# Kernel tuning notes

Hardware: AMD Instinct MI355X
Metric: run time of the kernel (lower is better)

## Reference

```python
import jax, jax.numpy as jnp
import numpy as np

N_AGENTS = 512
OBS = 128          # embed_fc_input_size (args.obs_space)
INP = 656          # input_shape
HID = 64           # rnn_hidden_dim
LAT = 256          # latent_dim (hard-coded)
NH = 64            # NN_HIDDEN_SIZE (hard-coded)
VAR_FLOOR = 0.002
KL_W = 1e-4
H_W = 1e-4
SOFT_W = 1.0
BN_EPS = 1e-5
LOG2PI = float(np.log(2.0 * np.pi))


def _bn(x, g, b, axis):
    # BatchNorm1d in training mode: biased batch stats over `axis`
    m = x.mean(axis=axis, keepdims=True)
    v = x.var(axis=axis, keepdims=True)
    return g * (x - m) / jnp.sqrt(v + BN_EPS) + b


def setup_inputs() -> dict:
    key = jax.random.key(0)
    ks = jax.random.split(key, 12)
    s = 0.02  # small init so exp(log-var head) stays tame
    p = {}
    p["obs"] = jax.random.normal(ks[0], (N_AGENTS, INP), jnp.float32)
    p["hidden_state"] = jax.random.normal(ks[1], (N_AGENTS, HID), jnp.float32)
    p["eps"] = jax.random.normal(ks[2], (N_AGENTS, LAT), jnp.float32)

    def lin(k, din, dout):
        return jax.random.normal(k, (din, dout), jnp.float32) * s, jnp.zeros((dout,), jnp.float32)

    # embed_net: Linear(OBS,64) -> BN -> LeakyReLU -> Linear(64, 2*LAT)
    p["eW1"], p["eb1"] = lin(ks[3], OBS, NH)
    p["eg"], p["ebt"] = jnp.ones((NH,), jnp.float32), jnp.zeros((NH,), jnp.float32)
    p["eW2"], p["eb2"] = lin(ks[4], NH, 2 * LAT)
    # inference_net: Linear(HID+INP,64) -> BN -> LeakyReLU -> Linear(64, 2*LAT)
    p["iW1"], p["ib1"] = lin(ks[5], HID + INP, NH)
    p["ig"], p["ibt"] = jnp.ones((NH,), jnp.float32), jnp.zeros((NH,), jnp.float32)
    p["iW2"], p["ib2"] = lin(ks[6], NH, 2 * LAT)
    # dis_net: Linear(2*LAT,64) -> BN -> LeakyReLU -> Linear(64,1)
    p["dW1"], p["db1"] = lin(ks[7], 2 * LAT, NH)
    p["dg"], p["dbt"] = jnp.ones((NH,), jnp.float32), jnp.zeros((NH,), jnp.float32)
    p["dW2"], p["db2"] = lin(ks[8], NH, 1)
    return p


def reference(obs, hidden_state, eps,
              eW1, eb1, eg, ebt, eW2, eb2,
              iW1, ib1, ig, ibt, iW2, ib2,
              dW1, db1, dg, dbt, dW2, db2):
    n = N_AGENTS  # bs == 1 is hard-coded in the module
    # --- embed_net ---
    emb_in = obs[:, -OBS:]
    h = jax.nn.leaky_relu(_bn(emb_in @ eW1 + eb1, eg, ebt, axis=0))
    lat = h @ eW2 + eb2                       # [n, 2*LAT]
    mu = lat[:, :LAT]
    var = jnp.maximum(jnp.exp(lat[:, LAT:]), VAR_FLOOR)
    sig = jnp.sqrt(var)
    latent = mu + sig * eps                   # rsample

    # --- inference_net (h_in detached) ---
    inf_in = jnp.concatenate([jax.lax.stop_gradient(hidden_state), obs], axis=1)
    hi = jax.nn.leaky_relu(_bn(inf_in @ iW1 + ib1, ig, ibt, axis=0))
    li = hi @ iW2 + ib2
    mu_q = li[:, :LAT]
    var_q = jnp.maximum(jnp.exp(li[:, LAT:]), VAR_FLOOR)
    sig_q = jnp.sqrt(var_q)

    entropy = (0.5 + 0.5 * LOG2PI + jnp.log(sig)).sum(-1).mean()
    kl = (jnp.log(sig_q / sig) + (var + (mu - mu_q) ** 2) / (2.0 * var_q) - 0.5).sum(-1).mean()
    loss0 = jnp.minimum(entropy * H_W + kl * KL_W, 2000.0)
    ce_loss = jnp.log1p(jnp.exp(loss0))

    # --- vectorized ring-shift pairwise pass (replaces n_agents Python loop) ---
    shifts = jnp.arange(1, n + 1)                        # loop iterations 1..n
    idx = (jnp.arange(n)[None, :] - shifts[:, None]) % n  # [n_shifts, n]
    moved = latent[idx]                                   # [S, n, LAT]

    # mi: per-dim Normal(mu_j, sig_j).log_prob of shifted latents
    logp = -((moved - mu[None]) ** 2) / (2.0 * var[None]) - jnp.log(sig)[None] - 0.5 * LOG2PI
    mi = jnp.maximum(logp + 13.9, -13.9).sum(-1) / LAT    # [S, n]

    # dis_net on concat(latent_j, moved_{s,j}); BN stats per shift iteration (batch = n)
    pair = jnp.concatenate([jnp.broadcast_to(latent[None], (n, n, LAT)), moved], axis=-1)
    h1 = pair @ dW1 + db1                                 # [S, n, NH]
    h1 = jax.nn.leaky_relu(_bn(h1, dg, dbt, axis=1))
    dis = jnp.abs(h1 @ dW2 + db2)[..., 0]                 # [S, n]

    mi_cat = mi.reshape(1, -1)                            # shift-major, matches cat order
    dis_cat = dis.reshape(1, -1)

    mi_n = (mi_cat - mi_cat.min(1, keepdims=True)) / (mi_cat.max(1, keepdims=True) - mi_cat.min(1, keepdims=True) + 1e-12)
    dis_n = (dis_cat - dis_cat.min(1, keepdims=True)) / (dis_cat.max(1, keepdims=True) - dis_cat.min(1, keepdims=True) + 1e-12)

    dis_loss = -jnp.minimum(mi_n + dis_n, 1.0).sum() / n  # / bs / n_agents, bs=1
    dis_norm = jnp.abs(dis_n).sum(axis=1).sum() / n
    c_dis_loss = (dis_norm + SOFT_W * dis_loss) / n
    loss = ce_loss + c_dis_loss
    return loss, c_dis_loss, ce_loss
```

## Files before the change

kernel.cpp:

```cpp
#include <hip/hip_runtime.h>

#define LOG2PI_F 1.8378770664093453f

#define W_ENC_PRE 0
#define W_INF_PRE 32768
#define W_ACC     65536
#define W_FIN     65792
#define W_MIMM    65796
#define W_DSMM    66308
#define W_ENT     67332
#define W_KL      67588
#define W_LATENT  67844
#define W_RPC     198916
#define W_A       723204
#define W_B       755972
#define W_AT      788740
#define W_BT      821508
#define W_ALPHA   854276
#define W_BETA    887044
#define W_MI      919812
#define W_DIS     1181956

__global__ __launch_bounds__(256) void k_pre(
    const float* __restrict__ obs, const float* __restrict__ hid,
    const float* __restrict__ eW1, const float* __restrict__ iW1,
    float* __restrict__ enc_pre, float* __restrict__ inf_pre,
    float* __restrict__ acc) {
  __shared__ float x[2][720];
  __shared__ float pi[4][2][64];
  __shared__ float pe[4][2][64];
  const int t = threadIdx.x;
  const int i0 = blockIdx.x * 2;
#pragma unroll
  for (int r = 0; r < 2; ++r)
    for (int k = t; k < 720; k += 256)
      x[r][k] = (k < 64) ? hid[(i0 + r) * 64 + k] : obs[(i0 + r) * 656 + (k - 64)];
  __syncthreads();
  const int c = t & 63, q = t >> 6;
  {
    float a0 = 0.f, a1 = 0.f;
    const int k0 = q * 180;
    for (int k = k0; k < k0 + 180; ++k) {
      const float w = iW1[k * 64 + c];
      a0 = fmaf(x[0][k], w, a0);
      a1 = fmaf(x[1][k], w, a1);
    }
    pi[q][0][c] = a0;
    pi[q][1][c] = a1;
  }
  {
    float a0 = 0.f, a1 = 0.f;
    const int k0 = q * 32;
    for (int k = k0; k < k0 + 32; ++k) {
      const float w = eW1[k * 64 + c];
      a0 = fmaf(x[0][592 + k], w, a0);
      a1 = fmaf(x[1][592 + k], w, a1);
    }
    pe[q][0][c] = a0;
    pe[q][1][c] = a1;
  }
  __syncthreads();
  if (t < 128) {
    const int r = t >> 6, c2 = t & 63;
    const float s = pi[0][r][c2] + pi[1][r][c2] + pi[2][r][c2] + pi[3][r][c2];
    inf_pre[(i0 + r) * 64 + c2] = s;
    atomicAdd(&acc[128 + c2], s);
    atomicAdd(&acc[192 + c2], s * s);
  } else {
    const int r = (t >> 6) & 1, c2 = t & 63;
    const float s = pe[0][r][c2] + pe[1][r][c2] + pe[2][r][c2] + pe[3][r][c2];
    enc_pre[(i0 + r) * 64 + c2] = s;
    atomicAdd(&acc[c2], s);
    atomicAdd(&acc[64 + c2], s * s);
  }
}

__global__ __launch_bounds__(256) void k_lat(
    const float* __restrict__ enc_pre, const float* __restrict__ inf_pre,
    const float* __restrict__ acc, const float* __restrict__ eg,
    const float* __restrict__ ebt, const float* __restrict__ ig,
    const float* __restrict__ ibt, const float* __restrict__ eW2,
    const float* __restrict__ eb2, const float* __restrict__ iW2,
    const float* __restrict__ ib2, const float* __restrict__ eps,
    float* __restrict__ latent, float* __restrict__ rpc,
    float* __restrict__ ent_part, float* __restrict__ kl_part) {
  __shared__ float sc[2][64], sh[2][64];
  __shared__ float h[2][2][64];
  __shared__ float red[256];
  const int t = threadIdx.x;
  const int i0 = blockIdx.x * 2;
  if (t < 128) {
    const int w = t >> 6, c = t & 63;
    const float sum = acc[w * 128 + c], sq = acc[w * 128 + 64 + c];
    const float mean = sum * (1.f / 512.f);
    float var = sq * (1.f / 512.f) - mean * mean;
    var = fmaxf(var, 0.f);
    const float g = w ? ig[c] : eg[c];
    const float bt = w ? ibt[c] : ebt[c];
    const float scale = g * rsqrtf(var + 1e-5f);
    sc[w][c] = scale;
    sh[w][c] = bt - mean * scale;
  }
  __syncthreads();
  {
    const int w = t >> 7, r = (t >> 6) & 1, c = t & 63;
    const float* pre = w ? inf_pre : enc_pre;
    const float v = fmaf(pre[(i0 + r) * 64 + c], sc[w][c], sh[w][c]);
    h[w][r][c] = (v >= 0.f) ? v : 0.01f * v;
  }
  __syncthreads();
  float me[2] = {0.f, 0.f}, ve[2] = {0.f, 0.f};
  float mq[2] = {0.f, 0.f}, vq[2] = {0.f, 0.f};
  for (int c = 0; c < 64; ++c) {
    const float we1 = eW2[c * 512 + t], we2 = eW2[c * 512 + 256 + t];
    const float wi1 = iW2[c * 512 + t], wi2 = iW2[c * 512 + 256 + t];
#pragma unroll
    for (int r = 0; r < 2; ++r) {
      me[r] = fmaf(h[0][r][c], we1, me[r]);
      ve[r] = fmaf(h[0][r][c], we2, ve[r]);
      mq[r] = fmaf(h[1][r][c], wi1, mq[r]);
      vq[r] = fmaf(h[1][r][c], wi2, vq[r]);
    }
  }
  const float ebm = eb2[t], ebv = eb2[256 + t];
  const float ibm = ib2[t], ibv = ib2[256 + t];
  float ent_l = 0.f, kl_l = 0.f;
#pragma unroll
  for (int r = 0; r < 2; ++r) {
    const int i = i0 + r;
    const float m = me[r] + ebm;
    const float var = fmaxf(expf(ve[r] + ebv), 0.002f);
    const float lse = 0.5f * logf(var);
    const float sig = sqrtf(var);
    const float mqq = mq[r] + ibm;
    const float varq = fmaxf(expf(vq[r] + ibv), 0.002f);
    const float lsq = 0.5f * logf(varq);
    latent[i * 256 + t] = fmaf(sig, eps[i * 256 + t], m);
    const float r_ = sqrtf(0.5f / var);
    float4 o;
    o.x = r_;
    o.y = m * r_;
    o.z = 13.9f - 0.5f * LOG2PI_F - lse;
    o.w = 0.f;
    *(float4*)&rpc[(i * 256 + t) * 4] = o;
    ent_l += 0.5f + 0.5f * LOG2PI_F + lse;
    const float dmu = m - mqq;
    kl_l += lsq - lse + (var + dmu * dmu) * (0.5f / varq) - 0.5f;
  }
  red[t] = ent_l;
  __syncthreads();
  for (int o = 128; o; o >>= 1) {
    if (t < o) red[t] += red[t + o];
    __syncthreads();
  }
  if (t == 0) ent_part[blockIdx.x] = red[0];
  __syncthreads();
  red[t] = kl_l;
  __syncthreads();
  for (int o = 128; o; o >>= 1) {
    if (t < o) red[t] += red[t + o];
    __syncthreads();
  }
  if (t == 0) kl_part[blockIdx.x] = red[0];
}

__global__ __launch_bounds__(256) void k_AB(
    const float* __restrict__ latent, const float* __restrict__ dW1,
    float* __restrict__ A, float* __restrict__ B, float* __restrict__ At,
    float* __restrict__ Bt, float* __restrict__ fin) {
  if (blockIdx.x == 0 && threadIdx.x == 0) {
    fin[0] = 0.f;
    fin[1] = 0.f;
    ((unsigned*)fin)[2] = 0u;
  }
  __shared__ float ls[2][256];
  __shared__ float pA[4][2][64], pB[4][2][64];
  const int t = threadIdx.x;
  const int j0 = blockIdx.x * 2;
  ls[0][t] = latent[j0 * 256 + t];
  ls[1][t] = latent[(j0 + 1) * 256 + t];
  __syncthreads();
  const int c = t & 63, q = t >> 6;
  float aA0 = 0.f, aA1 = 0.f, aB0 = 0.f, aB1 = 0.f;
  const int k0 = q * 64;
  for (int k = k0; k < k0 + 64; ++k) {
    const float wA = dW1[k * 64 + c];
    const float wB = dW1[(256 + k) * 64 + c];
    aA0 = fmaf(ls[0][k], wA, aA0);
    aA1 = fmaf(ls[1][k], wA, aA1);
    aB0 = fmaf(ls[0][k], wB, aB0);
    aB1 = fmaf(ls[1][k], wB, aB1);
  }
  pA[q][0][c] = aA0;
  pA[q][1][c] = aA1;
  pB[q][0][c] = aB0;
  pB[q][1][c] = aB1;
  __syncthreads();
  if (t < 128) {
    const int r = t >> 6, c2 = t & 63;
    const float s = pA[0][r][c2] + pA[1][r][c2] + pA[2][r][c2] + pA[3][r][c2];
    A[(j0 + r) * 64 + c2] = s;
    At[c2 * 512 + j0 + r] = s;
  } else {
    const int r = (t >> 6) & 1, c2 = t & 63;
    const float s = pB[0][r][c2] + pB[1][r][c2] + pB[2][r][c2] + pB[3][r][c2];
    B[(j0 + r) * 64 + c2] = s;
    Bt[c2 * 512 + j0 + r] = s;
  }
}

__global__ __launch_bounds__(256) void k_cross(
    const float* __restrict__ At, const float* __restrict__ Bt,
    const float* __restrict__ dg, const float* __restrict__ dbt,
    float* __restrict__ alpha, float* __restrict__ beta) {
  __shared__ float a[512], bb[512];
  __shared__ float red[256];
  __shared__ float pc[4][64];
  const int t = threadIdx.x;
  const int c = blockIdx.x >> 3;
  const int s0 = (blockIdx.x & 7) * 64;
  const float a0 = At[c * 512 + t], a1 = At[c * 512 + 256 + t];
  const float b0 = Bt[c * 512 + t], b1 = Bt[c * 512 + 256 + t];
  a[t] = a0;
  a[t + 256] = a1;
  bb[t] = b0;
  bb[t + 256] = b1;
  red[t] = a0 + a1 + b0 + b1;
  __syncthreads();
  for (int o = 128; o; o >>= 1) {
    if (t < o) red[t] += red[t + o];
    __syncthreads();
  }
  const float S = red[0];
  __syncthreads();
  red[t] = a0 * a0 + a1 * a1 + b0 * b0 + b1 * b1;
  __syncthreads();
  for (int o = 128; o; o >>= 1) {
    if (t < o) red[t] += red[t + o];
    __syncthreads();
  }
  const float Q = red[0];
  const int sl = t & 63, part = t >> 6;
  const int s = s0 + sl;
  float cr = 0.f;
  for (int j = part * 128; j < part * 128 + 128; ++j)
    cr = fmaf(a[j], bb[(j - s - 1) & 511], cr);
  pc[part][sl] = cr;
  __syncthreads();
  if (t < 64) {
    const int ss = s0 + t;
    const float cross = pc[0][t] + pc[1][t] + pc[2][t] + pc[3][t];
    const float mean = S * (1.f / 512.f);
    const float var = (Q + 2.f * cross) * (1.f / 512.f) - mean * mean;
    const float gc = dg[c], bc = dbt[c];
    const float al = rsqrtf(var + 1e-5f) * gc;
    alpha[ss * 64 + c] = al;
    beta[ss * 64 + c] = bc - mean * al;
  }
}

__global__ __launch_bounds__(256) void k_mi(
    const float* __restrict__ latent, const float* __restrict__ rpc,
    float* __restrict__ mi, float2* __restrict__ miMM) {
  __shared__ float lats[64][65];
  __shared__ float rpcs[16 * 256];
  __shared__ float mt[64][17];
  __shared__ float fmn[256], fmx[256];
  const int t = threadIdx.x;
  const int jt = blockIdx.x & 31, pt = blockIdx.x >> 5;
  const int j0 = jt * 16, p0 = pt * 64;
  const int pl = t & 31, jg = t >> 5;
  float regL[16], regR[16];
#pragma unroll
  for (int i = 0; i < 16; ++i) {
    const int idx = t + i * 256;
    regL[i] = latent[(p0 + (idx >> 6)) * 256 + (idx & 63)];
    regR[i] = rpc[(j0 + (idx >> 8)) * 1024 + (idx & 255)];
  }
  float a00 = 0.f, a01 = 0.f, a10 = 0.f, a11 = 0.f;
  for (int kc = 0; kc < 4; ++kc) {
    __syncthreads();
#pragma unroll
    for (int i = 0; i < 16; ++i) {
      const int idx = t + i * 256;
      lats[idx >> 6][idx & 63] = regL[i];
      rpcs[idx] = regR[i];
    }
    __syncthreads();
    if (kc < 3) {
#pragma unroll
      for (int i = 0; i < 16; ++i) {
        const int idx = t + i * 256;
        regL[i] = latent[(p0 + (idx >> 6)) * 256 + (kc + 1) * 64 + (idx & 63)];
        regR[i] = rpc[(j0 + (idx >> 8)) * 1024 + (kc + 1) * 256 + (idx & 255)];
      }
    }
    const float4* rp0 = (const float4*)&rpcs[(jg * 2) * 256];
    const float4* rp1 = (const float4*)&rpcs[(jg * 2 + 1) * 256];
#pragma unroll 8
    for (int k = 0; k < 64; ++k) {
      const float l0 = lats[pl][k], l1 = lats[pl + 32][k];
      const float4 r0 = rp0[k];
      const float4 r1 = rp1[k];
      float v;
      v = fmaf(l0, r0.x, -r0.y);
      a00 += fmaxf(fmaf(-v, v, r0.z), -13.9f);
      v = fmaf(l1, r0.x, -r0.y);
      a01 += fmaxf(fmaf(-v, v, r0.z), -13.9f);
      v = fmaf(l0, r1.x, -r1.y);
      a10 += fmaxf(fmaf(-v, v, r1.z), -13.9f);
      v = fmaf(l1, r1.x, -r1.y);
      a11 += fmaxf(fmaf(-v, v, r1.z), -13.9f);
    }
  }
  a00 *= (1.f / 256.f);
  a01 *= (1.f / 256.f);
  a10 *= (1.f / 256.f);
  a11 *= (1.f / 256.f);
  __syncthreads();
  mt[pl][jg * 2] = a00;
  mt[pl + 32][jg * 2] = a01;
  mt[pl][jg * 2 + 1] = a10;
  mt[pl + 32][jg * 2 + 1] = a11;
  fmn[t] = fminf(fminf(a00, a01), fminf(a10, a11));
  fmx[t] = fmaxf(fmaxf(a00, a01), fmaxf(a10, a11));
  __syncthreads();
  for (int o = 128; o; o >>= 1) {
    if (t < o) {
      fmn[t] = fminf(fmn[t], fmn[t + o]);
      fmx[t] = fmaxf(fmx[t], fmx[t + o]);
    }
    __syncthreads();
  }
  if (t == 0) miMM[blockIdx.x] = make_float2(fmn[0], fmx[0]);
  for (int i = t; i < 1024; i += 256) {
    const int pr = i >> 4, jc = i & 15;
    mi[(p0 + pr) * 512 + (j0 + jc)] = mt[pr][jc];
  }
}

__global__ __launch_bounds__(256) void k_dis(
    const float* __restrict__ A, const float* __restrict__ B,
    const float* __restrict__ alpha, const float* __restrict__ beta,
    const float* __restrict__ dW2, const float* __restrict__ db2,
    float* __restrict__ dis, float2* __restrict__ dsMM) {
  __shared__ float As[8 * 66];
  __shared__ float Bs[64 * 66];
  __shared__ float als[71 * 66];
  __shared__ float bes[71 * 66];
  __shared__ float w2s[64];
  __shared__ float dt[64][9];
  __shared__ float fmn[256], fmx[256];
  const int t = threadIdx.x;
  const int jt = blockIdx.x & 63, pt = blockIdx.x >> 6;
  const int j0 = jt * 8, p0 = pt * 64;
  for (int idx = t; idx < 8 * 64; idx += 256)
    As[(idx >> 6) * 66 + (idx & 63)] = A[(j0 + (idx >> 6)) * 64 + (idx & 63)];
  for (int idx = t; idx < 64 * 64; idx += 256)
    Bs[(idx >> 6) * 66 + (idx & 63)] = B[(p0 + (idx >> 6)) * 64 + (idx & 63)];
  for (int idx = t; idx < 71 * 64; idx += 256) {
    const int r = idx >> 6, c = idx & 63;
    const int s = (j0 - p0 - 64 + r) & 511;
    als[r * 66 + c] = alpha[s * 64 + c];
    bes[r * 66 + c] = beta[s * 64 + c];
  }
  if (t < 64) w2s[t] = dW2[t];
  const float db2v = db2[0];
  __syncthreads();
  const int pl = t & 31, jg = t >> 5;
  const int rb0 = jg - pl + 63;
  const int rb1 = jg - pl + 31;
  float acc0 = 0.f, acc1 = 0.f;
  for (int c = 0; c < 64; c += 2) {
    const float2 av = *(const float2*)&As[jg * 66 + c];
    const float2 bv0 = *(const float2*)&Bs[pl * 66 + c];
    const float2 bv1 = *(const float2*)&Bs[(pl + 32) * 66 + c];
    const float2 al0 = *(const float2*)&als[rb0 * 66 + c];
    const float2 al1 = *(const float2*)&als[rb1 * 66 + c];
    const float2 be0 = *(const float2*)&bes[rb0 * 66 + c];
    const float2 be1 = *(const float2*)&bes[rb1 * 66 + c];
    const float2 w = *(const float2*)&w2s[c];
    float v;
    v = fmaf(av.x + bv0.x, al0.x, be0.x);
    v = (v >= 0.f) ? v : 0.01f * v;
    acc0 = fmaf(v, w.x, acc0);
    v = fmaf(av.y + bv0.y, al0.y, be0.y);
    v = (v >= 0.f) ? v : 0.01f * v;
    acc0 = fmaf(v, w.y, acc0);
    v = fmaf(av.x + bv1.x, al1.x, be1.x);
    v = (v >= 0.f) ? v : 0.01f * v;
    acc1 = fmaf(v, w.x, acc1);
    v = fmaf(av.y + bv1.y, al1.y, be1.y);
    v = (v >= 0.f) ? v : 0.01f * v;
    acc1 = fmaf(v, w.y, acc1);
  }
  acc0 = fabsf(acc0 + db2v);
  acc1 = fabsf(acc1 + db2v);
  dt[pl][jg] = acc0;
  dt[pl + 32][jg] = acc1;
  fmn[t] = fminf(acc0, acc1);
  fmx[t] = fmaxf(acc0, acc1);
  __syncthreads();
  for (int o = 128; o; o >>= 1) {
    if (t < o) {
      fmn[t] = fminf(fmn[t], fmn[t + o]);
      fmx[t] = fmaxf(fmx[t], fmx[t + o]);
    }
    __syncthreads();
  }
  if (t == 0) dsMM[blockIdx.x] = make_float2(fmn[0], fmx[0]);
  for (int idx = t; idx < 512; idx += 256) {
    const int pr = idx >> 3, jc = idx & 7;
    dis[(p0 + pr) * 512 + (j0 + jc)] = dt[pr][jc];
  }
}

__global__ __launch_bounds__(256) void k_sumfin(
    const float* __restrict__ mi, const float* __restrict__ dis,
    const float2* __restrict__ miMM, const float2* __restrict__ dsMM,
    float* __restrict__ fin, const float* __restrict__ ent_part,
    const float* __restrict__ kl_part, float* __restrict__ out) {
  __shared__ float red1[256], red2[256], red3[256], red4[256];
  __shared__ int lastflag;
  const int t = threadIdx.x;
  {
    const float2 v = miMM[t];
    const float2 w0 = dsMM[t], w1 = dsMM[t + 256];
    red1[t] = v.x;
    red2[t] = v.y;
    red3[t] = fminf(w0.x, w1.x);
    red4[t] = fmaxf(w0.y, w1.y);
  }
  __syncthreads();
  for (int o = 128; o; o >>= 1) {
    if (t < o) {
      red1[t] = fminf(red1[t], red1[t + o]);
      red2[t] = fmaxf(red2[t], red2[t + o]);
      red3[t] = fminf(red3[t], red3[t + o]);
      red4[t] = fmaxf(red4[t], red4[t + o]);
    }
    __syncthreads();
  }
  const float mi_mn = red1[0], mi_mx = red2[0];
  const float d_mn = red3[0], d_mx = red4[0];
  __syncthreads();
  const float inv_mi = 1.f / (mi_mx - mi_mn + 1e-12f);
  const float inv_d = 1.f / (d_mx - d_mn + 1e-12f);
  float s1 = 0.f, s2 = 0.f;
  for (int i = blockIdx.x * 256 + t; i < 512 * 512; i += 65536) {
    const float mn_ = (mi[i] - mi_mn) * inv_mi;
    const float dn_ = (dis[i] - d_mn) * inv_d;
    s1 += fminf(mn_ + dn_, 1.0f);
    s2 += dn_;
  }
  red1[t] = s1;
  red2[t] = s2;
  __syncthreads();
  for (int o = 128; o; o >>= 1) {
    if (t < o) {
      red1[t] += red1[t + o];
      red2[t] += red2[t + o];
    }
    __syncthreads();
  }
  if (t == 0) {
    atomicAdd(&fin[0], red1[0]);
    atomicAdd(&fin[1], red2[0]);
    __threadfence();
    const unsigned old = atomicAdd((unsigned*)&fin[2], 1u);
    lastflag = (old == 255u) ? 1 : 0;
  }
  __syncthreads();
  if (!lastflag) return;
  red1[t] = ent_part[t];
  red2[t] = kl_part[t];
  __syncthreads();
  for (int o = 128; o; o >>= 1) {
    if (t < o) {
      red1[t] += red1[t + o];
      red2[t] += red2[t + o];
    }
    __syncthreads();
  }
  if (t == 0) {
    const float S1 = atomicAdd(&fin[0], 0.f);
    const float S2 = atomicAdd(&fin[1], 0.f);
    const double entropy = (double)red1[0] / 512.0;
    const double kl = (double)red2[0] / 512.0;
    double l0 = entropy * 1e-4 + kl * 1e-4;
    if (l0 > 2000.0) l0 = 2000.0;
    const double ce = log1p(exp(l0));
    const double dis_loss = -(double)S1 / 512.0;
    const double dis_norm = (double)S2 / 512.0;
    const double c_dis = (dis_norm + dis_loss) / 512.0;
    out[0] = (float)(ce + c_dis);
    out[1] = (float)c_dis;
    out[2] = (float)ce;
  }
}

extern "C" void kernel_launch(void* const* d_in, const int* in_sizes, int n_in,
                              void* d_out, int out_size, void* d_ws,
                              size_t ws_size, hipStream_t stream) {
  (void)in_sizes;
  (void)n_in;
  (void)out_size;
  (void)ws_size;
  const float* obs = (const float*)d_in[0];
  const float* hid = (const float*)d_in[1];
  const float* eps = (const float*)d_in[2];
  const float* eW1 = (const float*)d_in[3];
  const float* eg = (const float*)d_in[5];
  const float* ebt = (const float*)d_in[6];
  const float* eW2 = (const float*)d_in[7];
  const float* eb2 = (const float*)d_in[8];
  const float* iW1 = (const float*)d_in[9];
  const float* ig = (const float*)d_in[11];
  const float* ibt = (const float*)d_in[12];
  const float* iW2 = (const float*)d_in[13];
  const float* ib2 = (const float*)d_in[14];
  const float* dW1 = (const float*)d_in[15];
  const float* dg = (const float*)d_in[17];
  const float* dbt = (const float*)d_in[18];
  const float* dW2 = (const float*)d_in[19];
  const float* db2 = (const float*)d_in[20];
  float* ws = (float*)d_ws;
  float* out = (float*)d_out;

  hipMemsetAsync(ws + W_ACC, 0, 256 * sizeof(float), stream);

  k_pre<<<256, 256, 0, stream>>>(obs, hid, eW1, iW1, ws + W_ENC_PRE,
                                 ws + W_INF_PRE, ws + W_ACC);
  k_lat<<<256, 256, 0, stream>>>(ws + W_ENC_PRE, ws + W_INF_PRE, ws + W_ACC, eg,
                                 ebt, ig, ibt, eW2, eb2, iW2, ib2, eps,
                                 ws + W_LATENT, ws + W_RPC, ws + W_ENT,
                                 ws + W_KL);
  k_AB<<<256, 256, 0, stream>>>(ws + W_LATENT, dW1, ws + W_A, ws + W_B,
                                ws + W_AT, ws + W_BT, ws + W_FIN);
  k_cross<<<512, 256, 0, stream>>>(ws + W_AT, ws + W_BT, dg, dbt, ws + W_ALPHA,
                                   ws + W_BETA);
  k_mi<<<256, 256, 0, stream>>>(ws + W_LATENT, ws + W_RPC, ws + W_MI,
                                (float2*)(ws + W_MIMM));
  k_dis<<<512, 256, 0, stream>>>(ws + W_A, ws + W_B, ws + W_ALPHA, ws + W_BETA,
                                 dW2, db2, ws + W_DIS, (float2*)(ws + W_DSMM));
  k_sumfin<<<256, 256, 0, stream>>>(ws + W_MI, ws + W_DIS,
                                    (const float2*)(ws + W_MIMM),
                                    (const float2*)(ws + W_DSMM), ws + W_FIN,
                                    ws + W_ENT, ws + W_KL, out);
}
```

Before: 201.2 us.

## Fuse all stages into one cooperative megakernel with grid syncs

Replaces seven separate kernel launches and a memset with a single cooperative kernel of 512 blocks. Stages are separated by grid.sync and each block handles one row or tile. This removes launch and inter-kernel gaps, and the final atomic last-block reduction is replaced by per-block partials reduced after a grid sync. The cost is grid-wide barrier overhead, and occupancy is capped by the requirement that all 512 blocks be co-resident (launch bounds of 2 blocks per CU, large shared array).

Result: slower. 617.0 us (+206.7%).

```diff
diff --git a/kernel.cpp b/kernel.cpp
--- a/kernel.cpp
+++ b/kernel.cpp
@@ -1,501 +1,500 @@
 #include <hip/hip_runtime.h>
+#include <hip/hip_cooperative_groups.h>
+
+namespace cg = cooperative_groups;
 
 #define LOG2PI_F 1.8378770664093453f
 
 #define W_ENC_PRE 0
 #define W_INF_PRE 32768
 #define W_ACC     65536
-#define W_FIN     65792
-#define W_MIMM    65796
-#define W_DSMM    66308
-#define W_ENT     67332
-#define W_KL      67588
-#define W_LATENT  67844
-#define W_RPC     198916
-#define W_A       723204
-#define W_B       755972
-#define W_AT      788740
-#define W_BT      821508
-#define W_ALPHA   854276
-#define W_BETA    887044
-#define W_MI      919812
-#define W_DIS     1181956
-
-__global__ __launch_bounds__(256) void k_pre(
-    const float* __restrict__ obs, const float* __restrict__ hid,
-    const float* __restrict__ eW1, const float* __restrict__ iW1,
-    float* __restrict__ enc_pre, float* __restrict__ inf_pre,
-    float* __restrict__ acc) {
-  __shared__ float x[2][720];
-  __shared__ float pi[4][2][64];
-  __shared__ float pe[4][2][64];
+#define W_ENT     65792
+#define W_KL      66304
+#define W_MIMM    66816
+#define W_DSMM    67840
+#define W_S1P     68864
+#define W_S2P     69376
+#define W_LATENT  69888
+#define W_RPC     200960
+#define W_A       725248
+#define W_B       758016
+#define W_AT      790784
+#define W_BT      823552
+#define W_ALPHA   856320
+#define W_BETA    889088
+#define W_MI      921856
+#define W_DIS     1184000
+
+struct Params {
+  const float *obs, *hid, *eps;
+  const float *eW1, *eg, *ebt, *eW2, *eb2;
+  const float *iW1, *ig, *ibt, *iW2, *ib2;
+  const float *dW1, *dg, *dbt, *dW2, *db2;
+  float* ws;
+  float* out;
+};
+
+__global__ __launch_bounds__(256, 2) void megak(Params p) {
+  __shared__ __align__(16) float sm[15276];
+  cg::grid_group grid = cg::this_grid();
   const int t = threadIdx.x;
-  const int i0 = blockIdx.x * 2;
-#pragma unroll
-  for (int r = 0; r < 2; ++r)
+  const int vb = blockIdx.x;
+  float* ws = p.ws;
+  float* acc = ws + W_ACC;
+
+  if (vb == 0) acc[t] = 0.f;
+  grid.sync();
+
+  {
+    float* xs = sm;
+    float* pi = sm + 720;
+    float* pe = sm + 976;
+    const int i = vb;
     for (int k = t; k < 720; k += 256)
-      x[r][k] = (k < 64) ? hid[(i0 + r) * 64 + k] : obs[(i0 + r) * 656 + (k - 64)];
-  __syncthreads();
-  const int c = t & 63, q = t >> 6;
-  {
-    float a0 = 0.f, a1 = 0.f;
-    const int k0 = q * 180;
-    for (int k = k0; k < k0 + 180; ++k) {
-      const float w = iW1[k * 64 + c];
-      a0 = fmaf(x[0][k], w, a0);
-      a1 = fmaf(x[1][k], w, a1);
-    }
-    pi[q][0][c] = a0;
-    pi[q][1][c] = a1;
-  }
-  {
-    float a0 = 0.f, a1 = 0.f;
-    const int k0 = q * 32;
-    for (int k = k0; k < k0 + 32; ++k) {
-      const float w = eW1[k * 64 + c];
-      a0 = fmaf(x[0][592 + k], w, a0);
-      a1 = fmaf(x[1][592 + k], w, a1);
-    }
-    pe[q][0][c] = a0;
-    pe[q][1][c] = a1;
-  }
-  __syncthreads();
-  if (t < 128) {
-    const int r = t >> 6, c2 = t & 63;
-    const float s = pi[0][r][c2] + pi[1][r][c2] + pi[2][r][c2] + pi[3][r][c2];
-    inf_pre[(i0 + r) * 64 + c2] = s;
-    atomicAdd(&acc[128 + c2], s);
-    atomicAdd(&acc[192 + c2], s * s);
-  } else {
-    const int r = (t >> 6) & 1, c2 = t & 63;
-    const float s = pe[0][r][c2] + pe[1][r][c2] + pe[2][r][c2] + pe[3][r][c2];
-    enc_pre[(i0 + r) * 64 + c2] = s;
-    atomicAdd(&acc[c2], s);
-    atomicAdd(&acc[64 + c2], s * s);
-  }
-}
-
-__global__ __launch_bounds__(256) void k_lat(
-    const float* __restrict__ enc_pre, const float* __restrict__ inf_pre,
-    const float* __restrict__ acc, const float* __restrict__ eg,
-    const float* __restrict__ ebt, const float* __restrict__ ig,
-    const float* __restrict__ ibt, const float* __restrict__ eW2,
-    const float* __restrict__ eb2, const float* __restrict__ iW2,
-    const float* __restrict__ ib2, const float* __restrict__ eps,
-    float* __restrict__ latent, float* __restrict__ rpc,
-    float* __restrict__ ent_part, float* __restrict__ kl_part) {
-  __shared__ float sc[2][64], sh[2][64];
-  __shared__ float h[2][2][64];
-  __shared__ float red[256];
-  const int t = threadIdx.x;
-  const int i0 = blockIdx.x * 2;
-  if (t < 128) {
-    const int w = t >> 6, c = t & 63;
-    const float sum = acc[w * 128 + c], sq = acc[w * 128 + 64 + c];
-    const float mean = sum * (1.f / 512.f);
-    float var = sq * (1.f / 512.f) - mean * mean;
-    var = fmaxf(var, 0.f);
-    const float g = w ? ig[c] : eg[c];
-    const float bt = w ? ibt[c] : ebt[c];
-    const float scale = g * rsqrtf(var + 1e-5f);
-    sc[w][c] = scale;
-    sh[w][c] = bt - mean * scale;
-  }
-  __syncthreads();
-  {
-    const int w = t >> 7, r = (t >> 6) & 1, c = t & 63;
-    const float* pre = w ? inf_pre : enc_pre;
-    const float v = fmaf(pre[(i0 + r) * 64 + c], sc[w][c], sh[w][c]);
-    h[w][r][c] = (v >= 0.f) ? v : 0.01f * v;
-  }
-  __syncthreads();
-  float me[2] = {0.f, 0.f}, ve[2] = {0.f, 0.f};
-  float mq[2] = {0.f, 0.f}, vq[2] = {0.f, 0.f};
-  for (int c = 0; c < 64; ++c) {
-    const float we1 = eW2[c * 512 + t], we2 = eW2[c * 512 + 256 + t];
-    const float wi1 = iW2[c * 512 + t], wi2 = iW2[c * 512 + 256 + t];
-#pragma unroll
-    for (int r = 0; r < 2; ++r) {
-      me[r] = fmaf(h[0][r][c], we1, me[r]);
-      ve[r] = fmaf(h[0][r][c], we2, ve[r]);
-      mq[r] = fmaf(h[1][r][c], wi1, mq[r]);
-      vq[r] = fmaf(h[1][r][c], wi2, vq[r]);
-    }
-  }
-  const float ebm = eb2[t], ebv = eb2[256 + t];
-  const float ibm = ib2[t], ibv = ib2[256 + t];
-  float ent_l = 0.f, kl_l = 0.f;
-#pragma unroll
-  for (int r = 0; r < 2; ++r) {
-    const int i = i0 + r;
-    const float m = me[r] + ebm;
-    const float var = fmaxf(expf(ve[r] + ebv), 0.002f);
+      xs[k] = (k < 64) ? p.hid[i * 64 + k] : p.obs[i * 656 + (k - 64)];
+    __syncthreads();
+    const int c = t & 63, q = t >> 6;
+    {
+      float a0 = 0.f;
+      const int k0 = q * 180;
+      for (int k = k0; k < k0 + 180; ++k)
+        a0 = fmaf(xs[k], p.iW1[k * 64 + c], a0);
+      pi[q * 64 + c] = a0;
+    }
+    {
+      float a0 = 0.f;
+      const int k0 = q * 32;
+      for (int k = k0; k < k0 + 32; ++k)
+        a0 = fmaf(xs[592 + k], p.eW1[k * 64 + c], a0);
+      pe[q * 64 + c] = a0;
+    }
+    __syncthreads();
+    if (t < 64) {
+      const float s = pi[t] + pi[64 + t] + pi[128 + t] + pi[192 + t];
+      (ws + W_INF_PRE)[i * 64 + t] = s;
+      atomicAdd(&acc[128 + t], s);
+      atomicAdd(&acc[192 + t], s * s);
+    } else if (t < 128) {
+      const int c2 = t - 64;
+      const float s = pe[c2] + pe[64 + c2] + pe[128 + c2] + pe[192 + c2];
+      (ws + W_ENC_PRE)[i * 64 + c2] = s;
+      atomicAdd(&acc[c2], s);
+      atomicAdd(&acc[64 + c2], s * s);
+    }
+  }
+  grid.sync();
+
+  {
+    float* sc = sm;
+    float* sh = sm + 128;
+    float* h2 = sm + 256;
+    float* red = sm + 384;
+    const int i = vb;
+    if (t < 128) {
+      const int w = t >> 6, c = t & 63;
+      const float sum = acc[w * 128 + c], sq = acc[w * 128 + 64 + c];
+      const float mean = sum * (1.f / 512.f);
+      float var = sq * (1.f / 512.f) - mean * mean;
+      var = fmaxf(var, 0.f);
+      const float g = w ? p.ig[c] : p.eg[c];
+      const float bt = w ? p.ibt[c] : p.ebt[c];
+      const float scale = g * rsqrtf(var + 1e-5f);
+      sc[w * 64 + c] = scale;
+      sh[w * 64 + c] = bt - mean * scale;
+    }
+    __syncthreads();
+    if (t < 128) {
+      const int w = t >> 6, c = t & 63;
+      const float* pre = w ? (ws + W_INF_PRE) : (ws + W_ENC_PRE);
+      const float v = fmaf(pre[i * 64 + c], sc[w * 64 + c], sh[w * 64 + c]);
+      h2[w * 64 + c] = (v >= 0.f) ? v : 0.01f * v;
+    }
+    __syncthreads();
+    float me = 0.f, ve = 0.f, mq = 0.f, vq = 0.f;
+    for (int c = 0; c < 64; ++c) {
+      const float he = h2[c], hq = h2[64 + c];
+      me = fmaf(he, p.eW2[c * 512 + t], me);
+      ve = fmaf(he, p.eW2[c * 512 + 256 + t], ve);
+      mq = fmaf(hq, p.iW2[c * 512 + t], mq);
+      vq = fmaf(hq, p.iW2[c * 512 + 256 + t], vq);
+    }
+    const float m = me + p.eb2[t];
+    const float var = fmaxf(expf(ve + p.eb2[256 + t]), 0.002f);
     const float lse = 0.5f * logf(var);
     const float sig = sqrtf(var);
-    const float mqq = mq[r] + ibm;
-    const float varq = fmaxf(expf(vq[r] + ibv), 0.002f);
+    const float mqq = mq + p.ib2[t];
+    const float varq = fmaxf(expf(vq + p.ib2[256 + t]), 0.002f);
     const float lsq = 0.5f * logf(varq);
-    latent[i * 256 + t] = fmaf(sig, eps[i * 256 + t], m);
+    (ws + W_LATENT)[i * 256 + t] = fmaf(sig, p.eps[i * 256 + t], m);
     const float r_ = sqrtf(0.5f / var);
     float4 o;
     o.x = r_;
     o.y = m * r_;
     o.z = 13.9f - 0.5f * LOG2PI_F - lse;
     o.w = 0.f;
-    *(float4*)&rpc[(i * 256 + t) * 4] = o;
-    ent_l += 0.5f + 0.5f * LOG2PI_F + lse;
+    *(float4*)&(ws + W_RPC)[(i * 256 + t) * 4] = o;
+    const float ent_l = 0.5f + 0.5f * LOG2PI_F + lse;
     const float dmu = m - mqq;
-    kl_l += lsq - lse + (var + dmu * dmu) * (0.5f / varq) - 0.5f;
-  }
-  red[t] = ent_l;
-  __syncthreads();
-  for (int o = 128; o; o >>= 1) {
-    if (t < o) red[t] += red[t + o];
-    __syncthreads();
-  }
-  if (t == 0) ent_part[blockIdx.x] = red[0];
-  __syncthreads();
-  red[t] = kl_l;
-  __syncthreads();
-  for (int o = 128; o; o >>= 1) {
-    if (t < o) red[t] += red[t + o];
-    __syncthreads();
-  }
-  if (t == 0) kl_part[blockIdx.x] = red[0];
-}
-
-__global__ __launch_bounds__(256) void k_AB(
-    const float* __restrict__ latent, const float* __restrict__ dW1,
-    float* __restrict__ A, float* __restrict__ B, float* __restrict__ At,
-    float* __restrict__ Bt, float* __restrict__ fin) {
-  if (blockIdx.x == 0 && threadIdx.x == 0) {
-    fin[0] = 0.f;
-    fin[1] = 0.f;
-    ((unsigned*)fin)[2] = 0u;
-  }
-  __shared__ float ls[2][256];
-  __shared__ float pA[4][2][64], pB[4][2][64];
-  const int t = threadIdx.x;
-  const int j0 = blockIdx.x * 2;
-  ls[0][t] = latent[j0 * 256 + t];
-  ls[1][t] = latent[(j0 + 1) * 256 + t];
-  __syncthreads();
-  const int c = t & 63, q = t >> 6;
-  float aA0 = 0.f, aA1 = 0.f, aB0 = 0.f, aB1 = 0.f;
-  const int k0 = q * 64;
-  for (int k = k0; k < k0 + 64; ++k) {
-    const float wA = dW1[k * 64 + c];
-    const float wB = dW1[(256 + k) * 64 + c];
-    aA0 = fmaf(ls[0][k], wA, aA0);
-    aA1 = fmaf(ls[1][k], wA, aA1);
-    aB0 = fmaf(ls[0][k], wB, aB0);
-    aB1 = fmaf(ls[1][k], wB, aB1);
-  }
-  pA[q][0][c] = aA0;
-  pA[q][1][c] = aA1;
-  pB[q][0][c] = aB0;
-  pB[q][1][c] = aB1;
-  __syncthreads();
-  if (t < 128) {
-    const int r = t >> 6, c2 = t & 63;
-    const float s = pA[0][r][c2] + pA[1][r][c2] + pA[2][r][c2] + pA[3][r][c2];
-    A[(j0 + r) * 64 + c2] = s;
-    At[c2 * 512 + j0 + r] = s;
-  } else {
-    const int r = (t >> 6) & 1, c2 = t & 63;
-    const float s = pB[0][r][c2] + pB[1][r][c2] + pB[2][r][c2] + pB[3][r][c2];
-    B[(j0 + r) * 64 + c2] = s;
-    Bt[c2 * 512 + j0 + r] = s;
-  }
-}
-
-__global__ __launch_bounds__(256) void k_cross(
-    const float* __restrict__ At, const float* __restrict__ Bt,
-    const float* __restrict__ dg, const float* __restrict__ dbt,
-    float* __restrict__ alpha, float* __restrict__ beta) {
-  __shared__ float a[512], bb[512];
-  __shared__ float red[256];
-  __shared__ float pc[4][64];
-  const int t = threadIdx.x;
-  const int c = blockIdx.x >> 3;
-  const int s0 = (blockIdx.x & 7) * 64;
-  const float a0 = At[c * 512 + t], a1 = At[c * 512 + 256 + t];
-  const float b0 = Bt[c * 512 + t], b1 = Bt[c * 512 + 256 + t];
-  a[t] = a0;
-  a[t + 256] = a1;
-  bb[t] = b0;
-  bb[t + 256] = b1;
-  red[t] = a0 + a1 + b0 + b1;
-  __syncthreads();
-  for (int o = 128; o; o >>= 1) {
-    if (t < o) red[t] += red[t + o];
-    __syncthreads();
-  }
-  const float S = red[0];
-  __syncthreads();
-  red[t] = a0 * a0 + a1 * a1 + b0 * b0 + b1 * b1;
-  __syncthreads();
-  for (int o = 128; o; o >>= 1) {
-    if (t < o) red[t] += red[t + o];
-    __syncthreads();
-  }
-  const float Q = red[0];
-  const int sl = t & 63, part = t >> 6;
-  const int s = s0 + sl;
-  float cr = 0.f;
-  for (int j = part * 128; j < part * 128 + 128; ++j)
-    cr = fmaf(a[j], bb[(j - s - 1) & 511], cr);
-  pc[part][sl] = cr;
-  __syncthreads();
-  if (t < 64) {
-    const int ss = s0 + t;
-    const float cross = pc[0][t] + pc[1][t] + pc[2][t] + pc[3][t];
-    const float mean = S * (1.f / 512.f);
-    const float var = (Q + 2.f * cross) * (1.f / 512.f) - mean * mean;
-    const float gc = dg[c], bc = dbt[c];
-    const float al = rsqrtf(var + 1e-5f) * gc;
-    alpha[ss * 64 + c] = al;
-    beta[ss * 64 + c] = bc - mean * al;
-  }
-}
-
-__global__ __launch_bounds__(256) void k_mi(
-    const float* __restrict__ latent, const float* __restrict__ rpc,
-    float* __restrict__ mi, float2* __restrict__ miMM) {
-  __shared__ float lats[64][65];
-  __shared__ float rpcs[16 * 256];
-  __shared__ float mt[64][17];
-  __shared__ float fmn[256], fmx[256];
-  const int t = threadIdx.x;
-  const int jt = blockIdx.x & 31, pt = blockIdx.x >> 5;
-  const int j0 = jt * 16, p0 = pt * 64;
-  const int pl = t & 31, jg = t >> 5;
-  float regL[16], regR[16];
-#pragma unroll
-  for (int i = 0; i < 16; ++i) {
-    const int idx = t + i * 256;
-    regL[i] = latent[(p0 + (idx >> 6)) * 256 + (idx & 63)];
-    regR[i] = rpc[(j0 + (idx >> 8)) * 1024 + (idx & 255)];
-  }
-  float a00 = 0.f, a01 = 0.f, a10 = 0.f, a11 = 0.f;
-  for (int kc = 0; kc < 4; ++kc) {
-    __syncthreads();
+    const float kl_l = lsq - lse + (var + dmu * dmu) * (0.5f / varq) - 0.5f;
+    red[t] = ent_l;
+    __syncthreads();
+    for (int o2 = 128; o2; o2 >>= 1) {
+      if (t < o2) red[t] += red[t + o2];
+      __syncthreads();
+    }
+    if (t == 0) (ws + W_ENT)[i] = red[0];
+    __syncthreads();
+    red[t] = kl_l;
+    __syncthreads();
+    for (int o2 = 128; o2; o2 >>= 1) {
+      if (t < o2) red[t] += red[t + o2];
+      __syncthreads();
+    }
+    if (t == 0) (ws + W_KL)[i] = red[0];
+  }
+  grid.sync();
+
+  {
+    float* ls = sm;
+    float* pA = sm + 256;
+    float* pB = sm + 512;
+    const int i = vb;
+    ls[t] = (ws + W_LATENT)[i * 256 + t];
+    __syncthreads();
+    const int c = t & 63, q = t >> 6;
+    float aA = 0.f, aB = 0.f;
+    const int k0 = q * 64;
+    for (int k = k0; k < k0 + 64; ++k) {
+      const float x = ls[k];
+      aA = fmaf(x, p.dW1[k * 64 + c], aA);
+      aB = fmaf(x, p.dW1[(256 + k) * 64 + c], aB);
+    }
+    pA[q * 64 + c] = aA;
+    pB[q * 64 + c] = aB;
+    __syncthreads();
+    if (t < 64) {
+      const float s = pA[t] + pA[64 + t] + pA[128 + t] + pA[192 + t];
+      (ws + W_A)[i * 64 + t] = s;
+      (ws + W_AT)[t * 512 + i] = s;
+    } else if (t < 128) {
+      const int c2 = t - 64;
+      const float s = pB[c2] + pB[64 + c2] + pB[128 + c2] + pB[192 + c2];
+      (ws + W_B)[i * 64 + c2] = s;
+      (ws + W_BT)[c2 * 512 + i] = s;
+    }
+  }
+  grid.sync();
+
+  {
+    float* a = sm;
+    float* bb = sm + 512;
+    float* red = sm + 1024;
+    float* pc = sm + 1280;
+    const int c = vb >> 3;
+    const int s0 = (vb & 7) * 64;
+    const float* At = ws + W_AT;
+    const float* Bt = ws + W_BT;
+    const float a0 = At[c * 512 + t], a1 = At[c * 512 + 256 + t];
+    const float b0 = Bt[c * 512 + t], b1 = Bt[c * 512 + 256 + t];
+    a[t] = a0;
+    a[t + 256] = a1;
+    bb[t] = b0;
+    bb[t + 256] = b1;
+    red[t] = a0 + a1 + b0 + b1;
+    __syncthreads();
+    for (int o = 128; o; o >>= 1) {
+      if (t < o) red[t] += red[t + o];
+      __syncthreads();
+    }
+    const float S = red[0];
+    __syncthreads();
+    red[t] = a0 * a0 + a1 * a1 + b0 * b0 + b1 * b1;
+    __syncthreads();
+    for (int o = 128; o; o >>= 1) {
+      if (t < o) red[t] += red[t + o];
+      __syncthreads();
+    }
+    const float Q = red[0];
+    const int sl = t & 63, part = t >> 6;
+    const int s = s0 + sl;
+    float cr = 0.f;
+    for (int j = part * 128; j < part * 128 + 128; ++j)
+      cr = fmaf(a[j], bb[(j - s - 1) & 511], cr);
+    pc[part * 64 + sl] = cr;
+    __syncthreads();
+    if (t < 64) {
+      const int ss = s0 + t;
+      const float cross = pc[t] + pc[64 + t] + pc[128 + t] + pc[192 + t];
+      const float mean = S * (1.f / 512.f);
+      const float var = (Q + 2.f * cross) * (1.f / 512.f) - mean * mean;
+      const float gc = p.dg[c], bc = p.dbt[c];
+      const float al = rsqrtf(var + 1e-5f) * gc;
+      (ws + W_ALPHA)[ss * 64 + c] = al;
+      (ws + W_BETA)[ss * 64 + c] = bc - mean * al;
+    }
+  }
+  grid.sync();
+
+  {
+    float* lats = sm;
+    float* rpcs = sm + 4160;
+    float* mt = sm + 6208;
+    float* fmn = sm + 6784;
+    float* fmx = sm + 7040;
+    const int jt = vb & 63, pt = vb >> 6;
+    const int j0 = jt * 8, p0 = pt * 64;
+    const int pl = t & 31, jg = t >> 5;
+    const float* latent = ws + W_LATENT;
+    const float* rpc = ws + W_RPC;
+    float regL[16], regR[8];
 #pragma unroll
     for (int i = 0; i < 16; ++i) {
       const int idx = t + i * 256;
-      lats[idx >> 6][idx & 63] = regL[i];
-      rpcs[idx] = regR[i];
-    }
-    __syncthreads();
-    if (kc < 3) {
+      regL[i] = latent[(p0 + (idx >> 6)) * 256 + (idx & 63)];
+    }
+#pragma unroll
+    for (int i = 0; i < 8; ++i) {
+      const int idx = t + i * 256;
+      regR[i] = rpc[(j0 + (idx >> 8)) * 1024 + (idx & 255)];
+    }
+    float a00 = 0.f, a01 = 0.f;
+    for (int kc = 0; kc < 4; ++kc) {
+      __syncthreads();
 #pragma unroll
       for (int i = 0; i < 16; ++i) {
         const int idx = t + i * 256;
-        regL[i] = latent[(p0 + (idx >> 6)) * 256 + (kc + 1) * 64 + (idx & 63)];
-        regR[i] = rpc[(j0 + (idx >> 8)) * 1024 + (kc + 1) * 256 + (idx & 255)];
-      }
-    }
-    const float4* rp0 = (const float4*)&rpcs[(jg * 2) * 256];
-    const float4* rp1 = (const float4*)&rpcs[(jg * 2 + 1) * 256];
+        lats[(idx >> 6) * 65 + (idx & 63)] = regL[i];
+      }
+#pragma unroll
+      for (int i = 0; i < 8; ++i) rpcs[t + i * 256] = regR[i];
+      __syncthreads();
+      if (kc < 3) {
+#pragma unroll
+        for (int i = 0; i < 16; ++i) {
+          const int idx = t + i * 256;
+          regL[i] = latent[(p0 + (idx >> 6)) * 256 + (kc + 1) * 64 + (idx & 63)];
+        }
+#pragma unroll
+        for (int i = 0; i < 8; ++i) {
+          const int idx = t + i * 256;
+          regR[i] = rpc[(j0 + (idx >> 8)) * 1024 + (kc + 1) * 256 + (idx & 255)];
+        }
+      }
+      const float4* rp0 = (const float4*)&rpcs[jg * 256];
 #pragma unroll 8
-    for (int k = 0; k < 64; ++k) {
-      const float l0 = lats[pl][k], l1 = lats[pl + 32][k];
-      const float4 r0 = rp0[k];
-      const float4 r1 = rp1[k];
+      for (int k = 0; k < 64; ++k) {
+        const float l0 = lats[pl * 65 + k], l1 = lats[(pl + 32) * 65 + k];
+        const float4 r0 = rp0[k];
+        float v;
+        v = fmaf(l0, r0.x, -r0.y);
+        a00 += fmaxf(fmaf(-v, v, r0.z), -13.9f);
+        v = fmaf(l1, r0.x, -r0.y);
+        a01 += fmaxf(fmaf(-v, v, r0.z), -13.9f);
+      }
+    }
+    a00 *= (1.f / 256.f);
+    a01 *= (1.f / 256.f);
+    __syncthreads();
+    mt[pl * 9 + jg] = a00;
+    mt[(pl + 32) * 9 + jg] = a01;
+    fmn[t] = fminf(a00, a01);
+    fmx[t] = fmaxf(a00, a01);
+    __syncthreads();
+    for (int o = 128; o; o >>= 1) {
+      if (t < o) {
+        fmn[t] = fminf(fmn[t], fmn[t + o]);
+        fmx[t] = fmaxf(fmx[t], fmx[t + o]);
+      }
+      __syncthreads();
+    }
+    if (t == 0) ((float2*)(ws + W_MIMM))[vb] = make_float2(fmn[0], fmx[0]);
+    float* mi = ws + W_MI;
+    for (int i = t; i < 512; i += 256) {
+      const int pr = i >> 3, jc = i & 7;
+      mi[(p0 + pr) * 512 + (j0 + jc)] = mt[pr * 9 + jc];
+    }
+  }
+  grid.sync();
+
+  {
+    float* As = sm;
+    float* Bs = sm + 528;
+    float* als = sm + 4752;
+    float* bes = sm + 9438;
+    float* w2s = sm + 14124;
+    float* dt = sm + 14188;
+    float* fmn = sm + 14764;
+    float* fmx = sm + 15020;
+    const int jt = vb & 63, pt = vb >> 6;
+    const int j0 = jt * 8, p0 = pt * 64;
+    const float* A = ws + W_A;
+    const float* B = ws + W_B;
+    const float* alpha = ws + W_ALPHA;
+    const float* beta = ws + W_BETA;
+    for (int idx = t; idx < 8 * 64; idx += 256)
+      As[(idx >> 6) * 66 + (idx & 63)] = A[(j0 + (idx >> 6)) * 64 + (idx & 63)];
+    for (int idx = t; idx < 64 * 64; idx += 256)
+      Bs[(idx >> 6) * 66 + (idx & 63)] = B[(p0 + (idx >> 6)) * 64 + (idx & 63)];
+    for (int idx = t; idx < 71 * 64; idx += 256) {
+      const int r = idx >> 6, c = idx & 63;
+      const int s = (j0 - p0 - 64 + r) & 511;
+      als[r * 66 + c] = alpha[s * 64 + c];
+      bes[r * 66 + c] = beta[s * 64 + c];
+    }
+    if (t < 64) w2s[t] = p.dW2[t];
+    const float db2v = p.db2[0];
+    __syncthreads();
+    const int pl = t & 31, jg = t >> 5;
+    const int rb0 = jg - pl + 63;
+    const int rb1 = jg - pl + 31;
+    float acc0 = 0.f, acc1 = 0.f;
+    for (int c = 0; c < 64; c += 2) {
+      const float2 av = *(const float2*)&As[jg * 66 + c];
+      const float2 bv0 = *(const float2*)&Bs[pl * 66 + c];
+      const float2 bv1 = *(const float2*)&Bs[(pl + 32) * 66 + c];
+      const float2 al0 = *(const float2*)&als[rb0 * 66 + c];
+      const float2 al1 = *(const float2*)&als[rb1 * 66 + c];
+      const float2 be0 = *(const float2*)&bes[rb0 * 66 + c];
+      const float2 be1 = *(const float2*)&bes[rb1 * 66 + c];
+      const float2 w = *(const float2*)&w2s[c];
       float v;
-      v = fmaf(l0, r0.x, -r0.y);
-      a00 += fmaxf(fmaf(-v, v, r0.z), -13.9f);
-      v = fmaf(l1, r0.x, -r0.y);
-      a01 += fmaxf(fmaf(-v, v, r0.z), -13.9f);
-      v = fmaf(l0, r1.x, -r1.y);
-      a10 += fmaxf(fmaf(-v, v, r1.z), -13.9f);
-      v = fmaf(l1, r1.x, -r1.y);
-      a11 += fmaxf(fmaf(-v, v, r1.z), -13.9f);
-    }
-  }
-  a00 *= (1.f / 256.f);
-  a01 *= (1.f / 256.f);
-  a10 *= (1.f / 256.f);
-  a11 *= (1.f / 256.f);
-  __syncthreads();
-  mt[pl][jg * 2] = a00;
-  mt[pl + 32][jg * 2] = a01;
-  mt[pl][jg * 2 + 1] = a10;
-  mt[pl + 32][jg * 2 + 1] = a11;
-  fmn[t] = fminf(fminf(a00, a01), fminf(a10, a11));
-  fmx[t] = fmaxf(fmaxf(a00, a01), fmaxf(a10, a11));
-  __syncthreads();
-  for (int o = 128; o; o >>= 1) {
-    if (t < o) {
-      fmn[t] = fminf(fmn[t], fmn[t + o]);
-      fmx[t] = fmaxf(fmx[t], fmx[t + o]);
-    }
-    __syncthreads();
-  }
-  if (t == 0) miMM[blockIdx.x] = make_float2(fmn[0], fmx[0]);
-  for (int i = t; i < 1024; i += 256) {
-    const int pr = i >> 4, jc = i & 15;
-    mi[(p0 + pr) * 512 + (j0 + jc)] = mt[pr][jc];
-  }
-}
-
-__global__ __launch_bounds__(256) void k_dis(
-    const float* __restrict__ A, const float* __restrict__ B,
-    const float* __restrict__ alpha, const float* __restrict__ beta,
-    const float* __restrict__ dW2, const float* __restrict__ db2,
-    float* __restrict__ dis, float2* __restrict__ dsMM) {
-  __shared__ float As[8 * 66];
-  __shared__ float Bs[64 * 66];
-  __shared__ float als[71 * 66];
-  __shared__ float bes[71 * 66];
-  __shared__ float w2s[64];
-  __shared__ float dt[64][9];
-  __shared__ float fmn[256], fmx[256];
-  const int t = threadIdx.x;
-  const int jt = blockIdx.x & 63, pt = blockIdx.x >> 6;
-  const int j0 = jt * 8, p0 = pt * 64;
-  for (int idx = t; idx < 8 * 64; idx += 256)
-    As[(idx >> 6) * 66 + (idx & 63)] = A[(j0 + (idx >> 6)) * 64 + (idx & 63)];
-  for (int idx = t; idx < 64 * 64; idx += 256)
-    Bs[(idx >> 6) * 66 + (idx & 63)] = B[(p0 + (idx >> 6)) * 64 + (idx & 63)];
-  for (int idx = t; idx < 71 * 64; idx += 256) {
-    const int r = idx >> 6, c = idx & 63;
-    const int s = (j0 - p0 - 64 + r) & 511;
-    als[r * 66 + c] = alpha[s * 64 + c];
-    bes[r * 66 + c] = beta[s * 64 + c];
-  }
-  if (t < 64) w2s[t] = dW2[t];
-  const float db2v = db2[0];
-  __syncthreads();
-  const int pl = t & 31, jg = t >> 5;
-  const int rb0 = jg - pl + 63;
-  const int rb1 = jg - pl + 31;
-  float acc0 = 0.f, acc1 = 0.f;
-  for (int c = 0; c < 64; c += 2) {
-    const float2 av = *(const float2*)&As[jg * 66 + c];
-    const float2 bv0 = *(const float2*)&Bs[pl * 66 + c];
-    const float2 bv1 = *(const float2*)&Bs[(pl + 32) * 66 + c];
-    const float2 al0 = *(const float2*)&als[rb0 * 66 + c];
-    const float2 al1 = *(const float2*)&als[rb1 * 66 + c];
-    const float2 be0 = *(const float2*)&bes[rb0 * 66 + c];
-    const float2 be1 = *(const float2*)&bes[rb1 * 66 + c];
-    const float2 w = *(const float2*)&w2s[c];
-    float v;
-    v = fmaf(av.x + bv0.x, al0.x, be0.x);
-    v = (v >= 0.f) ? v : 0.01f * v;
-    acc0 = fmaf(v, w.x, acc0);
-    v = fmaf(av.y + bv0.y, al0.y, be0.y);
-    v = (v >= 0.f) ? v : 0.01f * v;
-    acc0 = fmaf(v, w.y, acc0);
-    v = fmaf(av.x + bv1.x, al1.x, be1.x);
-    v = (v >= 0.f) ? v : 0.01f * v;
-    acc1 = fmaf(v, w.x, acc1);
-    v = fmaf(av.y + bv1.y, al1.y, be1.y);
-    v = (v >= 0.f) ? v : 0.01f * v;
-    acc1 = fmaf(v, w.y, acc1);
-  }
-  acc0 = fabsf(acc0 + db2v);
-  acc1 = fabsf(acc1 + db2v);
-  dt[pl][jg] = acc0;
-  dt[pl + 32][jg] = acc1;
-  fmn[t] = fminf(acc0, acc1);
-  fmx[t] = fmaxf(acc0, acc1);
-  __syncthreads();
-  for (int o = 128; o; o >>= 1) {
-    if (t < o) {
-      fmn[t] = fminf(fmn[t], fmn[t + o]);
-      fmx[t] = fmaxf(fmx[t], fmx[t + o]);
-    }
-    __syncthreads();
-  }
-  if (t == 0) dsMM[blockIdx.x] = make_float2(fmn[0], fmx[0]);
-  for (int idx = t; idx < 512; idx += 256) {
-    const int pr = idx >> 3, jc = idx & 7;
-    dis[(p0 + pr) * 512 + (j0 + jc)] = dt[pr][jc];
-  }
-}
-
-__global__ __launch_bounds__(256) void k_sumfin(
-    const float* __restrict__ mi, const float* __restrict__ dis,
-    const float2* __restrict__ miMM, const float2* __restrict__ dsMM,
-    float* __restrict__ fin, const float* __restrict__ ent_part,
-    const float* __restrict__ kl_part, float* __restrict__ out) {
-  __shared__ float red1[256], red2[256], red3[256], red4[256];
-  __shared__ int lastflag;
-  const int t = threadIdx.x;
-  {
-    const float2 v = miMM[t];
-    const float2 w0 = dsMM[t], w1 = dsMM[t + 256];
-    red1[t] = v.x;
-    red2[t] = v.y;
-    red3[t] = fminf(w0.x, w1.x);
-    red4[t] = fmaxf(w0.y, w1.y);
-  }
-  __syncthreads();
-  for (int o = 128; o; o >>= 1) {
-    if (t < o) {
-      red1[t] = fminf(red1[t], red1[t + o]);
-      red2[t] = fmaxf(red2[t], red2[t + o]);
-      red3[t] = fminf(red3[t], red3[t + o]);
-      red4[t] = fmaxf(red4[t], red4[t + o]);
-    }
-    __syncthreads();
-  }
-  const float mi_mn = red1[0], mi_mx = red2[0];
-  const float d_mn = red3[0], d_mx = red4[0];
-  __syncthreads();
-  const float inv_mi = 1.f / (mi_mx - mi_mn + 1e-12f);
-  const float inv_d = 1.f / (d_mx - d_mn + 1e-12f);
-  float s1 = 0.f, s2 = 0.f;
-  for (int i = blockIdx.x * 256 + t; i < 512 * 512; i += 65536) {
-    const float mn_ = (mi[i] - mi_mn) * inv_mi;
-    const float dn_ = (dis[i] - d_mn) * inv_d;
-    s1 += fminf(mn_ + dn_, 1.0f);
-    s2 += dn_;
-  }
-  red1[t] = s1;
-  red2[t] = s2;
-  __syncthreads();
-  for (int o = 128; o; o >>= 1) {
-    if (t < o) {
-      red1[t] += red1[t + o];
-      red2[t] += red2[t + o];
-    }
-    __syncthreads();
-  }
-  if (t == 0) {
-    atomicAdd(&fin[0], red1[0]);
-    atomicAdd(&fin[1], red2[0]);
-    __threadfence();
-    const unsigned old = atomicAdd((unsigned*)&fin[2], 1u);
-    lastflag = (old == 255u) ? 1 : 0;
-  }
-  __syncthreads();
-  if (!lastflag) return;
-  red1[t] = ent_part[t];
-  red2[t] = kl_part[t];
-  __syncthreads();
-  for (int o = 128; o; o >>= 1) {
-    if (t < o) {
-      red1[t] += red1[t + o];
-      red2[t] += red2[t + o];
-    }
-    __syncthreads();
-  }
-  if (t == 0) {
-    const float S1 = atomicAdd(&fin[0], 0.f);
-    const float S2 = atomicAdd(&fin[1], 0.f);
-    const double entropy = (double)red1[0] / 512.0;
-    const double kl = (double)red2[0] / 512.0;
-    double l0 = entropy * 1e-4 + kl * 1e-4;
-    if (l0 > 2000.0) l0 = 2000.0;
-    const double ce = log1p(exp(l0));
-    const double dis_loss = -(double)S1 / 512.0;
-    const double dis_norm = (double)S2 / 512.0;
-    const double c_dis = (dis_norm + dis_loss) / 512.0;
-    out[0] = (float)(ce + c_dis);
-    out[1] = (float)c_dis;
-    out[2] = (float)ce;
+      v = fmaf(av.x + bv0.x, al0.x, be0.x);
+      v = (v >= 0.f) ? v : 0.01f * v;
+      acc0 = fmaf(v, w.x, acc0);
+      v = fmaf(av.y + bv0.y, al0.y, be0.y);
+      v = (v >= 0.f) ? v : 0.01f * v;
+      acc0 = fmaf(v, w.y, acc0);
+      v = fmaf(av.x + bv1.x, al1.x, be1.x);
+      v = (v >= 0.f) ? v : 0.01f * v;
+      acc1 = fmaf(v, w.x, acc1);
+      v = fmaf(av.y + bv1.y, al1.y, be1.y);
+      v = (v >= 0.f) ? v : 0.01f * v;
+      acc1 = fmaf(v, w.y, acc1);
+    }
+    acc0 = fabsf(acc0 + db2v);
+    acc1 = fabsf(acc1 + db2v);
+    dt[pl * 9 + jg] = acc0;
+    dt[(pl + 32) * 9 + jg] = acc1;
+    fmn[t] = fminf(acc0, acc1);
+    fmx[t] = fmaxf(acc0, acc1);
+    __syncthreads();
+    for (int o = 128; o; o >>= 1) {
+      if (t < o) {
+        fmn[t] = fminf(fmn[t], fmn[t + o]);
+        fmx[t] = fmaxf(fmx[t], fmx[t + o]);
+      }
+      __syncthreads();
+    }
+    if (t == 0) ((float2*)(ws + W_DSMM))[vb] = make_float2(fmn[0], fmx[0]);
+    float* dis = ws + W_DIS;
+    for (int i = t; i < 512; i += 256) {
+      const int pr = i >> 3, jc = i & 7;
+      dis[(p0 + pr) * 512 + (j0 + jc)] = dt[pr * 9 + jc];
+    }
+  }
+  grid.sync();
+
+  {
+    float* red1 = sm;
+    float* red2 = sm + 256;
+    float* red3 = sm + 512;
+    float* red4 = sm + 768;
+    const float2* miMM = (const float2*)(ws + W_MIMM);
+    const float2* dsMM = (const float2*)(ws + W_DSMM);
+    const float2 m0 = miMM[t], m1 = miMM[t + 256];
+    const float2 d0 = dsMM[t], d1 = dsMM[t + 256];
+    red1[t] = fminf(m0.x, m1.x);
+    red2[t] = fmaxf(m0.y, m1.y);
+    red3[t] = fminf(d0.x, d1.x);
+    red4[t] = fmaxf(d0.y, d1.y);
+    __syncthreads();
+    for (int o = 128; o; o >>= 1) {
+      if (t < o) {
+        red1[t] = fminf(red1[t], red1[t + o]);
+        red2[t] = fmaxf(red2[t], red2[t + o]);
+        red3[t] = fminf(red3[t], red3[t + o]);
+        red4[t] = fmaxf(red4[t], red4[t + o]);
+      }
+      __syncthreads();
+    }
+    const float mi_mn = red1[0], mi_mx = red2[0];
+    const float d_mn = red3[0], d_mx = red4[0];
+    __syncthreads();
+    const float inv_mi = 1.f / (mi_mx - mi_mn + 1e-12f);
+    const float inv_d = 1.f / (d_mx - d_mn + 1e-12f);
+    const float* mi = ws + W_MI;
+    const float* dis = ws + W_DIS;
+    float s1 = 0.f, s2 = 0.f;
+    for (int i = vb * 256 + t; i < 512 * 512; i += 131072) {
+      const float mn_ = (mi[i] - mi_mn) * inv_mi;
+      const float dn_ = (dis[i] - d_mn) * inv_d;
+      s1 += fminf(mn_ + dn_, 1.0f);
+      s2 += dn_;
+    }
+    red1[t] = s1;
+    red2[t] = s2;
+    __syncthreads();
+    for (int o = 128; o; o >>= 1) {
+      if (t < o) {
+        red1[t] += red1[t + o];
+        red2[t] += red2[t + o];
+      }
+      __syncthreads();
+    }
+    if (t == 0) {
+      (ws + W_S1P)[vb] = red1[0];
+      (ws + W_S2P)[vb] = red2[0];
+    }
+  }
+  grid.sync();
+
+  if (vb == 0) {
+    double* redd = (double*)sm;
+    double S1, S2, E, K;
+    redd[t] = (double)(ws + W_S1P)[t] + (double)(ws + W_S1P)[t + 256];
+    __syncthreads();
+    for (int o = 128; o; o >>= 1) {
+      if (t < o) redd[t] += redd[t + o];
+      __syncthreads();
+    }
+    S1 = redd[0];
+    __syncthreads();
+    redd[t] = (double)(ws + W_S2P)[t] + (double)(ws + W_S2P)[t + 256];
+    __syncthreads();
+    for (int o = 128; o; o >>= 1) {
+      if (t < o) redd[t] += redd[t + o];
+      __syncthreads();
+    }
+    S2 = redd[0];
+    __syncthreads();
+    redd[t] = (double)(ws + W_ENT)[t] + (double)(ws + W_ENT)[t + 256];
+    __syncthreads();
+    for (int o = 128; o; o >>= 1) {
+      if (t < o) redd[t] += redd[t + o];
+      __syncthreads();
+    }
+    E = redd[0];
+    __syncthreads();
+    redd[t] = (double)(ws + W_KL)[t] + (double)(ws + W_KL)[t + 256];
+    __syncthreads();
+    for (int o = 128; o; o >>= 1) {
+      if (t < o) redd[t] += redd[t + o];
+      __syncthreads();
+    }
+    K = redd[0];
+    if (t == 0) {
+      const double entropy = E / 512.0;
+      const double kl = K / 512.0;
+      double l0 = entropy * 1e-4 + kl * 1e-4;
+      if (l0 > 2000.0) l0 = 2000.0;
+      const double ce = log1p(exp(l0));
+      const double dis_loss = -S1 / 512.0;
+      const double dis_norm = S2 / 512.0;
+      const double c_dis = (dis_norm + dis_loss) / 512.0;
+      p.out[0] = (float)(ce + c_dis);
+      p.out[1] = (float)c_dis;
+      p.out[2] = (float)ce;
+    }
   }
 }
 
@@ -506,45 +505,29 @@
   (void)n_in;
   (void)out_size;
   (void)ws_size;
-  const float* obs = (const float*)d_in[0];
-  const float* hid = (const float*)d_in[1];
-  const float* eps = (const float*)d_in[2];
-  const float* eW1 = (const float*)d_in[3];
-  const float* eg = (const float*)d_in[5];
-  const float* ebt = (const float*)d_in[6];
-  const float* eW2 = (const float*)d_in[7];
-  const float* eb2 = (const float*)d_in[8];
-  const float* iW1 = (const float*)d_in[9];
-  const float* ig = (const float*)d_in[11];
-  const float* ibt = (const float*)d_in[12];
-  const float* iW2 = (const float*)d_in[13];
-  const float* ib2 = (const float*)d_in[14];
-  const float* dW1 = (const float*)d_in[15];
-  const float* dg = (const float*)d_in[17];
-  const float* dbt = (const float*)d_in[18];
-  const float* dW2 = (const float*)d_in[19];
-  const float* db2 = (const float*)d_in[20];
-  float* ws = (float*)d_ws;
-  float* out = (float*)d_out;
-
-  hipMemsetAsync(ws + W_ACC, 0, 256 * sizeof(float), stream);
-
-  k_pre<<<256, 256, 0, stream>>>(obs, hid, eW1, iW1, ws + W_ENC_PRE,
-                                 ws + W_INF_PRE, ws + W_ACC);
-  k_lat<<<256, 256, 0, stream>>>(ws + W_ENC_PRE, ws + W_INF_PRE, ws + W_ACC, eg,
-                                 ebt, ig, ibt, eW2, eb2, iW2, ib2, eps,
-                                 ws + W_LATENT, ws + W_RPC, ws + W_ENT,
-                                 ws + W_KL);
-  k_AB<<<256, 256, 0, stream>>>(ws + W_LATENT, dW1, ws + W_A, ws + W_B,
-                                ws + W_AT, ws + W_BT, ws + W_FIN);
-  k_cross<<<512, 256, 0, stream>>>(ws + W_AT, ws + W_BT, dg, dbt, ws + W_ALPHA,
-                                   ws + W_BETA);
-  k_mi<<<256, 256, 0, stream>>>(ws + W_LATENT, ws + W_RPC, ws + W_MI,
-                                (float2*)(ws + W_MIMM));
-  k_dis<<<512, 256, 0, stream>>>(ws + W_A, ws + W_B, ws + W_ALPHA, ws + W_BETA,
-                                 dW2, db2, ws + W_DIS, (float2*)(ws + W_DSMM));
-  k_sumfin<<<256, 256, 0, stream>>>(ws + W_MI, ws + W_DIS,
-                                    (const float2*)(ws + W_MIMM),
-                                    (const float2*)(ws + W_DSMM), ws + W_FIN,
-                                    ws + W_ENT, ws + W_KL, out);
+  Params prm;
+  prm.obs = (const float*)d_in[0];
+  prm.hid = (const float*)d_in[1];
+  prm.eps = (const float*)d_in[2];
+  prm.eW1 = (const float*)d_in[3];
+  prm.eg = (const float*)d_in[5];
+  prm.ebt = (const float*)d_in[6];
+  prm.eW2 = (const float*)d_in[7];
+  prm.eb2 = (const float*)d_in[8];
+  prm.iW1 = (const float*)d_in[9];
+  prm.ig = (const float*)d_in[11];
+  prm.ibt = (const float*)d_in[12];
+  prm.iW2 = (const float*)d_in[13];
+  prm.ib2 = (const float*)d_in[14];
+  prm.dW1 = (const float*)d_in[15];
+  prm.dg = (const float*)d_in[17];
+  prm.dbt = (const float*)d_in[18];
+  prm.dW2 = (const float*)d_in[19];
+  prm.db2 = (const float*)d_in[20];
+  prm.ws = (float*)d_ws;
+  prm.out = (float*)d_out;
+
+  void* args[] = {&prm};
+  hipLaunchCooperativeKernel((const void*)megak, dim3(512), dim3(256), args, 0,
+                             stream);
 }
```
